# Performance work log

Measured on AMD Instinct MI355X. Metric: run time of the kernel, lower is better.

## Reference

```python
import jax, jax.numpy as jnp
import numpy as np

B, S, E, H, DQ = 8, 1024, 128, 8, 128  # batch, seq, embedding_dim, head_num, qkv_dim
HD = H * DQ  # 1024


def setup_inputs() -> dict:
    key = jax.random.key(0)
    ks = jax.random.split(key, 8)
    q = jax.random.normal(ks[0], (B, S, E), dtype=jnp.float32)
    k = jax.random.normal(ks[1], (B, S, E), dtype=jnp.float32)
    v = jax.random.normal(ks[2], (B, S, E), dtype=jnp.float32)
    mask = jnp.zeros((B, S), dtype=jnp.float32)  # rank2 ninf mask (additive)
    scale = 0.02
    Wq = jax.random.normal(ks[3], (HD, E), dtype=jnp.float32) * scale  # torch Linear weight [out,in]
    Wk = jax.random.normal(ks[4], (HD, E), dtype=jnp.float32) * scale
    Wv = jax.random.normal(ks[5], (HD, E), dtype=jnp.float32) * scale
    Wc = jax.random.normal(ks[6], (E, HD), dtype=jnp.float32) * scale
    bc = jax.random.normal(ks[7], (E,), dtype=jnp.float32) * scale
    return {"q": q, "k": k, "v": v, "mask": mask,
            "Wq": Wq, "Wk": Wk, "Wv": Wv, "Wc": Wc, "bc": bc}


def reference(q, k, v, mask, Wq, Wk, Wv, Wc, bc):
    batch, n, emb = q.shape
    hd = Wq.shape[0]
    # Faithful to source quirk: head_num recomputed as out_features // in_features
    head_num = hd // emb
    BIG = 1e9
    EPS = 1e-12

    def heads(x):  # [B, n, HD] -> [B, H, n, d]
        return x.reshape(batch, -1, head_num, hd // head_num).transpose(0, 2, 1, 3)

    qh = heads(q @ Wq.T)
    kh = heads(k @ Wk.T)
    vh = heads(v @ Wv.T)
    d = qh.shape[-1]

    score = jnp.einsum('bhnd,bhmd->bhnm', qh, kh) / jnp.sqrt(jnp.float32(d))
    score = score + mask[:, None, None, :]
    score = jnp.nan_to_num(score, nan=-BIG, posinf=BIG, neginf=-BIG)
    w = jax.nn.softmax(score, axis=-1)
    w = jnp.nan_to_num(w, nan=0.0, posinf=0.0, neginf=0.0)
    w = jnp.maximum(w, 0.0)
    row_sum = jnp.sum(w, axis=-1, keepdims=True)
    # zero-row fallback: replace fully-masked rows with tiny uniform weights
    w = jnp.where(row_sum <= 0.0, EPS, w)
    row_sum = jnp.sum(w, axis=-1, keepdims=True)
    w = w / (row_sum + EPS)

    out = jnp.einsum('bhnm,bhmd->bhnd', w, vh)  # [B,H,n,d]
    out_concat = out.transpose(0, 2, 1, 3).reshape(batch, n, hd)
    return out_concat @ Wc.T + bc
```

## Files before the change

kernel.cpp:

```cpp
#include <hip/hip_runtime.h>

typedef __bf16 bf16;
typedef __attribute__((ext_vector_type(8))) __bf16 bf16x8;
typedef __attribute__((ext_vector_type(4))) __bf16 bf16x4;
typedef __attribute__((ext_vector_type(4))) float f32x4;

constexpr int Bb = 8;
constexpr int Ss = 1024;
constexpr int Ee = 128;
constexpr int Hh = 8;
constexpr int Dd = 128;
constexpr int HD = 1024;

__device__ __forceinline__ void gl_lds16(const bf16* gp, bf16* lp) {
    __builtin_amdgcn_global_load_lds(
        (const __attribute__((address_space(1))) unsigned int*)gp,
        (__attribute__((address_space(3))) unsigned int*)lp, 16, 0, 0);
}

__global__ void k_cvt(const float* __restrict__ Wq, const float* __restrict__ Wk,
                      const float* __restrict__ Wv,
                      bf16* __restrict__ Wqb, bf16* __restrict__ Wkb, bf16* __restrict__ Wvb)
{
    int gid = blockIdx.x * 256 + threadIdx.x;
    const float* src; bf16* dst; int off; float s = 1.0f;
    if      (gid < 32768) { src = Wq; dst = Wqb; off = gid;         s = 0.12751741530603157f; }
    else if (gid < 65536) { src = Wk; dst = Wkb; off = gid - 32768; }
    else                  { src = Wv; dst = Wvb; off = gid - 65536; }
    float4 f = ((const float4*)src)[off];
    bf16x4 p;
    p[0] = (bf16)(f.x * s); p[1] = (bf16)(f.y * s);
    p[2] = (bf16)(f.z * s); p[3] = (bf16)(f.w * s);
    ((bf16x4*)dst)[off] = p;
}

__global__ __launch_bounds__(256, 2) void k_qkv(
    const float* __restrict__ qin, const float* __restrict__ kin, const float* __restrict__ vin,
    const bf16* __restrict__ Wqb, const bf16* __restrict__ Wkb, const bf16* __restrict__ Wvb,
    bf16* __restrict__ Qh, bf16* __restrict__ Kh, bf16* __restrict__ Vt)
{
    const int rb    = blockIdx.x;
    const int h     = blockIdx.y;
    const int which = blockIdx.z;
    const float* x = (which == 0) ? qin : (which == 1) ? kin : vin;
    const bf16*  W = (which == 0) ? Wqb : (which == 1) ? Wkb : Wvb;

    __shared__ bf16 Xs[128][136];
    __shared__ bf16 Ws[128][136];

    const int tid  = threadIdx.x;
    const int wv   = tid >> 6;
    const int lane = tid & 63;
    const int lo   = lane & 15;
    const int q4   = lane >> 4;

#pragma unroll
    for (int t = 0; t < 8; ++t) {
        int c = tid + t * 256;
        int row = c >> 4, c8 = (c & 15) << 3;
        const float* xp = &x[(rb * 128 + row) * Ee + c8];
        float4 f0 = *(const float4*)xp;
        float4 f1 = *(const float4*)(xp + 4);
        bf16x8 p;
        p[0] = (bf16)f0.x; p[1] = (bf16)f0.y; p[2] = (bf16)f0.z; p[3] = (bf16)f0.w;
        p[4] = (bf16)f1.x; p[5] = (bf16)f1.y; p[6] = (bf16)f1.z; p[7] = (bf16)f1.w;
        *(bf16x8*)&Xs[row][c8] = p;
        *(bf16x8*)&Ws[row][c8] = *(const bf16x8*)&W[(h * 128 + row) * Ee + c8];
    }
    __syncthreads();

    const bf16 (*Ap)[136] = (which == 2) ? Ws : Xs;
    const bf16 (*Bp)[136] = (which == 2) ? Xs : Ws;

    f32x4 acc[2][8];
#pragma unroll
    for (int i = 0; i < 2; ++i)
#pragma unroll
        for (int j = 0; j < 8; ++j) acc[i][j] = f32x4{0.f, 0.f, 0.f, 0.f};

#pragma unroll
    for (int kq = 0; kq < 4; ++kq) {
        bf16x8 a[2], b8[8];
#pragma unroll
        for (int ri = 0; ri < 2; ++ri)
            a[ri] = *(const bf16x8*)&Ap[wv * 32 + ri * 16 + lo][kq * 32 + q4 * 8];
#pragma unroll
        for (int cj = 0; cj < 8; ++cj)
            b8[cj] = *(const bf16x8*)&Bp[cj * 16 + lo][kq * 32 + q4 * 8];
#pragma unroll
        for (int ri = 0; ri < 2; ++ri)
#pragma unroll
            for (int cj = 0; cj < 8; ++cj)
                acc[ri][cj] = __builtin_amdgcn_mfma_f32_16x16x32_bf16(
                    a[ri], b8[cj], acc[ri][cj], 0, 0, 0);
    }

    const int bb = rb >> 3;
    const int s0 = (rb & 7) * 128;
    if (which < 2) {
        bf16* dst = ((which == 0) ? Qh : Kh) + (bb * Hh + h) * Ss * Dd;
#pragma unroll
        for (int ri = 0; ri < 2; ++ri)
#pragma unroll
            for (int cj = 0; cj < 8; ++cj)
#pragma unroll
                for (int r = 0; r < 4; ++r) {
                    int row = wv * 32 + ri * 16 + q4 * 4 + r;
                    int col = cj * 16 + lo;
                    dst[(s0 + row) * Dd + col] = (bf16)acc[ri][cj][r];
                }
    } else {
        bf16* dst = Vt + (bb * Hh + h) * Dd * Ss;
#pragma unroll
        for (int ri = 0; ri < 2; ++ri)
#pragma unroll
            for (int cj = 0; cj < 8; ++cj)
#pragma unroll
                for (int r = 0; r < 4; ++r) {
                    int row = wv * 32 + ri * 16 + q4 * 4 + r;
                    int col = cj * 16 + lo;
                    dst[row * Ss + s0 + col] = (bf16)acc[ri][cj][r];
                }
    }
}

__global__ __launch_bounds__(512, 2) void k_attn(
    const bf16* __restrict__ Qh, const bf16* __restrict__ Kh, const bf16* __restrict__ Vt,
    const float* __restrict__ mask, bf16* __restrict__ oc)
{
    const int bh = blockIdx.x;
    const int qg = blockIdx.y;
    const int b  = bh >> 3;
    const int h  = bh & 7;
    const int tid  = threadIdx.x;
    const int wv   = tid >> 6;
    const int lane = tid & 63;
    const int lo   = lane & 15;
    const int q4   = lane >> 4;

    __shared__ bf16 KsL[2][64 * 128];
    __shared__ bf16 VsL[2][128 * 64];
    __shared__ float maskS[1024];

    const bf16* Qb = Qh + bh * Ss * Dd;
    const bf16* Kb = Kh + bh * Ss * Dd;
    const bf16* Vb = Vt + bh * Dd * Ss;

    auto stage = [&](int bi, int j0) {
#pragma unroll
        for (int t = 0; t < 2; ++t) {
            int i = wv * 2 + t;
            int row = i * 4 + (lane >> 4);
            int grow = (row & 32) + (((row >> 2) & 3) << 3)
                     + (((row >> 4) & 1) << 2) + (row & 3);
            int g = (lane & 15) ^ (row & 7);
            gl_lds16(Kb + (j0 + grow) * Dd + g * 8, &KsL[bi][i * 512]);
        }
#pragma unroll
        for (int t = 0; t < 2; ++t) {
            int i = wv * 2 + t;
            int row = i * 8 + (lane >> 3);
            int g = (lane & 7) ^ (row & 7);
            gl_lds16(Vb + row * Ss + j0 + g * 8, &VsL[bi][i * 512]);
        }
    };

    stage(0, 0);

#pragma unroll
    for (int t = 0; t < 2; ++t)
        maskS[tid + t * 512] = mask[b * Ss + tid + t * 512] * 1.4426950408889634f;

    const int q0 = qg * 256 + wv * 32;
    bf16x8 qf[2][4];
#pragma unroll
    for (int nt = 0; nt < 2; ++nt)
#pragma unroll
        for (int kq = 0; kq < 4; ++kq)
            qf[nt][kq] = *(const bf16x8*)&Qb[(q0 + nt * 16 + lo) * Dd + kq * 32 + q4 * 8];

    f32x4 accO[8][2];
#pragma unroll
    for (int dm = 0; dm < 8; ++dm)
#pragma unroll
        for (int nt = 0; nt < 2; ++nt) accO[dm][nt] = f32x4{0.f, 0.f, 0.f, 0.f};
    float lsum[2] = {0.f, 0.f};

    const int sw = lo & 7;

#pragma unroll 2
    for (int kt = 0; kt < 16; ++kt) {
        const int bi = kt & 1;
        const int j0 = kt * 64;
        __syncthreads();
        if (kt < 15) stage(bi ^ 1, j0 + 64);

        f32x4 sc[4][2];
#pragma unroll
        for (int c = 0; c < 4; ++c)
#pragma unroll
            for (int nt = 0; nt < 2; ++nt) sc[c][nt] = f32x4{0.f, 0.f, 0.f, 0.f};
#pragma unroll
        for (int kq = 0; kq < 4; ++kq) {
            bf16x8 kf[4];
#pragma unroll
            for (int c = 0; c < 4; ++c)
                kf[c] = *(const bf16x8*)&KsL[bi][(c * 16 + lo) * 128 + (((kq << 2) + q4) ^ sw) * 8];
#pragma unroll
            for (int c = 0; c < 4; ++c)
#pragma unroll
                for (int nt = 0; nt < 2; ++nt)
                    sc[c][nt] = __builtin_amdgcn_mfma_f32_16x16x32_bf16(
                        kf[c], qf[nt][kq], sc[c][nt], 0, 0, 0);
        }

        bf16x8 p8[2][2];
#pragma unroll
        for (int kb = 0; kb < 2; ++kb) {
#pragma unroll
            for (int t = 0; t < 2; ++t) {
                const float4 mv = *(const float4*)&maskS[j0 + kb * 32 + q4 * 8 + t * 4];
                const int c = kb * 2 + t;
#pragma unroll
                for (int nt = 0; nt < 2; ++nt) {
                    float e0 = exp2f(sc[c][nt][0] + mv.x);
                    float e1 = exp2f(sc[c][nt][1] + mv.y);
                    float e2 = exp2f(sc[c][nt][2] + mv.z);
                    float e3 = exp2f(sc[c][nt][3] + mv.w);
                    lsum[nt] += (e0 + e1) + (e2 + e3);
                    p8[kb][nt][t * 4 + 0] = (bf16)e0;
                    p8[kb][nt][t * 4 + 1] = (bf16)e1;
                    p8[kb][nt][t * 4 + 2] = (bf16)e2;
                    p8[kb][nt][t * 4 + 3] = (bf16)e3;
                }
            }
        }

#pragma unroll
        for (int kb = 0; kb < 2; ++kb)
#pragma unroll
            for (int dm = 0; dm < 8; ++dm) {
                bf16x8 vf = *(const bf16x8*)&VsL[bi][(dm * 16 + lo) * 64 + (((kb << 2) + q4) ^ sw) * 8];
#pragma unroll
                for (int nt = 0; nt < 2; ++nt)
                    accO[dm][nt] = __builtin_amdgcn_mfma_f32_16x16x32_bf16(
                        vf, p8[kb][nt], accO[dm][nt], 0, 0, 0);
            }
    }

#pragma unroll
    for (int nt = 0; nt < 2; ++nt) {
        float s = lsum[nt];
        s += __shfl_xor(s, 16, 64);
        s += __shfl_xor(s, 32, 64);
        float inv = 1.0f / (s + 1e-12f);
        int sg = q0 + nt * 16 + lo;
        bf16* dst = oc + (b * Ss + sg) * HD + h * 128;
#pragma unroll
        for (int dm = 0; dm < 8; ++dm) {
            bf16x4 o;
#pragma unroll
            for (int r = 0; r < 4; ++r) o[r] = (bf16)(accO[dm][nt][r] * inv);
            *(bf16x4*)&dst[dm * 16 + q4 * 4] = o;
        }
    }
}

__global__ __launch_bounds__(256, 4) void k_proj(
    const bf16* __restrict__ oc, const float* __restrict__ Wc,
    const float* __restrict__ bc, float* __restrict__ out)
{
    const int mt   = blockIdx.x;
    const int tid  = threadIdx.x;
    const int wv   = tid >> 6;
    const int lane = tid & 63;
    const int lo   = lane & 15;
    const int q4   = lane >> 4;

    f32x4 acc[2];
    acc[0] = f32x4{0.f, 0.f, 0.f, 0.f};
    acc[1] = f32x4{0.f, 0.f, 0.f, 0.f};

    const bf16* arow = oc + (mt * 16 + lo) * HD + q4 * 8;

    for (int kc = 0; kc < 8; ++kc) {
        const int k0 = kc * 128;
        bf16x8 a[4];
#pragma unroll
        for (int kq = 0; kq < 4; ++kq)
            a[kq] = *(const bf16x8*)&arow[k0 + kq * 32];
#pragma unroll
        for (int cj = 0; cj < 2; ++cj) {
            const int n = wv * 32 + cj * 16 + lo;
#pragma unroll
            for (int kq = 0; kq < 4; ++kq) {
                const float* wp = &Wc[n * HD + k0 + kq * 32 + q4 * 8];
                float4 f0 = *(const float4*)wp;
                float4 f1 = *(const float4*)(wp + 4);
                bf16x8 bfr;
                bfr[0] = (bf16)f0.x; bfr[1] = (bf16)f0.y; bfr[2] = (bf16)f0.z; bfr[3] = (bf16)f0.w;
                bfr[4] = (bf16)f1.x; bfr[5] = (bf16)f1.y; bfr[6] = (bf16)f1.z; bfr[7] = (bf16)f1.w;
                acc[cj] = __builtin_amdgcn_mfma_f32_16x16x32_bf16(
                    a[kq], bfr, acc[cj], 0, 0, 0);
            }
        }
    }

#pragma unroll
    for (int cj = 0; cj < 2; ++cj) {
        int col = wv * 32 + cj * 16 + lo;
        float bias = bc[col];
#pragma unroll
        for (int r = 0; r < 4; ++r) {
            int row = mt * 16 + q4 * 4 + r;
            out[row * Ee + col] = acc[cj][r] + bias;
        }
    }
}

extern "C" void kernel_launch(void* const* d_in, const int* in_sizes, int n_in,
                              void* d_out, int out_size, void* d_ws, size_t ws_size,
                              hipStream_t stream)
{
    const float* q    = (const float*)d_in[0];
    const float* k    = (const float*)d_in[1];
    const float* v    = (const float*)d_in[2];
    const float* mask = (const float*)d_in[3];
    const float* Wq   = (const float*)d_in[4];
    const float* Wk   = (const float*)d_in[5];
    const float* Wv   = (const float*)d_in[6];
    const float* Wc   = (const float*)d_in[7];
    const float* bc   = (const float*)d_in[8];
    float* out = (float*)d_out;

    constexpr int NBH = Bb * Hh * Ss * Dd;
    bf16* Qh = (bf16*)d_ws;
    bf16* Kh = Qh + NBH;
    bf16* Vt = Kh + NBH;
    bf16* oc = Vt + NBH;
    bf16* Wqb = oc;
    bf16* Wkb = Wqb + HD * Ee;
    bf16* Wvb = Wkb + HD * Ee;

    k_cvt<<<dim3(384), 256, 0, stream>>>(Wq, Wk, Wv, Wqb, Wkb, Wvb);
    k_qkv<<<dim3(64, 8, 3), 256, 0, stream>>>(q, k, v, Wqb, Wkb, Wvb, Qh, Kh, Vt);
    k_attn<<<dim3(64, 4), 512, 0, stream>>>(Qh, Kh, Vt, mask, oc);
    k_proj<<<dim3(512), 256, 0, stream>>>(oc, Wc, bc, out);
}
```

Before: 178.4 us.

## Shrink attention blocks to 2 waves and 32-key tiles with new LDS swizzle

Restructures the attention kernel from 512-thread blocks covering 256 queries to 128-thread blocks covering 64 queries, launching 1024 blocks instead of 256. Key/value tiles shrink from 64 to 32 keys per iteration, giving 32 iterations, with a new XOR swizzle pattern and precomputed staging offsets. The aim is more blocks in flight across CUs and less LDS per block. In exchange, each K/V tile is reused by fewer waves, so global traffic for K/V rises fourfold, and there are twice as many barriers per block.

```diff
diff --git a/kernel.cpp b/kernel.cpp
--- a/kernel.cpp
+++ b/kernel.cpp
@@ -124,7 +124,7 @@
     }
 }
 
-__global__ __launch_bounds__(512, 2) void k_attn(
+__global__ __launch_bounds__(128, 2) void k_attn(
     const bf16* __restrict__ Qh, const bf16* __restrict__ Kh, const bf16* __restrict__ Vt,
     const float* __restrict__ mask, bf16* __restrict__ oc)
 {
@@ -138,40 +138,43 @@
     const int lo   = lane & 15;
     const int q4   = lane >> 4;
 
-    __shared__ bf16 KsL[2][64 * 128];
-    __shared__ bf16 VsL[2][128 * 64];
+    __shared__ bf16 KsL[2][32 * 128];
+    __shared__ bf16 VsL[2][128 * 32];
     __shared__ float maskS[1024];
 
     const bf16* Qb = Qh + bh * Ss * Dd;
     const bf16* Kb = Kh + bh * Ss * Dd;
     const bf16* Vb = Vt + bh * Dd * Ss;
 
+    int koff[4], voff[4];
+#pragma unroll
+    for (int t = 0; t < 4; ++t) {
+        int i = wv * 4 + t;
+        int rho  = i * 4 + (lane >> 4);
+        int kap  = 8 * ((rho >> 2) & 3) + 4 * ((rho >> 4) & 1) + (rho & 3);
+        int sK   = ((((rho >> 1) ^ (rho >> 3)) & 1) << 2) | (((rho >> 2) & 1) << 3);
+        int gK   = (lane & 15) ^ sK;
+        koff[t]  = kap * Dd + gK * 8;
+        int vrow = i * 16 + (lane >> 2);
+        voff[t]  = vrow * Ss + (lane & 3) * 8;
+    }
+
     auto stage = [&](int bi, int j0) {
 #pragma unroll
-        for (int t = 0; t < 2; ++t) {
-            int i = wv * 2 + t;
-            int row = i * 4 + (lane >> 4);
-            int grow = (row & 32) + (((row >> 2) & 3) << 3)
-                     + (((row >> 4) & 1) << 2) + (row & 3);
-            int g = (lane & 15) ^ (row & 7);
-            gl_lds16(Kb + (j0 + grow) * Dd + g * 8, &KsL[bi][i * 512]);
-        }
-#pragma unroll
-        for (int t = 0; t < 2; ++t) {
-            int i = wv * 2 + t;
-            int row = i * 8 + (lane >> 3);
-            int g = (lane & 7) ^ (row & 7);
-            gl_lds16(Vb + row * Ss + j0 + g * 8, &VsL[bi][i * 512]);
-        }
+        for (int t = 0; t < 4; ++t)
+            gl_lds16(Kb + j0 * Dd + koff[t], &KsL[bi][(wv * 4 + t) * 512]);
+#pragma unroll
+        for (int t = 0; t < 4; ++t)
+            gl_lds16(Vb + j0 + voff[t], &VsL[bi][(wv * 4 + t) * 512]);
     };
 
     stage(0, 0);
 
 #pragma unroll
-    for (int t = 0; t < 2; ++t)
-        maskS[tid + t * 512] = mask[b * Ss + tid + t * 512] * 1.4426950408889634f;
-
-    const int q0 = qg * 256 + wv * 32;
+    for (int t = 0; t < 8; ++t)
+        maskS[tid + t * 128] = mask[b * Ss + tid + t * 128] * 1.4426950408889634f;
+
+    const int q0 = qg * 64 + wv * 32;
     bf16x8 qf[2][4];
 #pragma unroll
     for (int nt = 0; nt < 2; ++nt)
@@ -186,66 +189,60 @@
         for (int nt = 0; nt < 2; ++nt) accO[dm][nt] = f32x4{0.f, 0.f, 0.f, 0.f};
     float lsum[2] = {0.f, 0.f};
 
-    const int sw = lo & 7;
+    const int sw2 = ((((lo >> 1) ^ (lo >> 3)) & 1) << 2) | (((lo >> 2) & 1) << 3);
 
 #pragma unroll 2
-    for (int kt = 0; kt < 16; ++kt) {
+    for (int kt = 0; kt < 32; ++kt) {
         const int bi = kt & 1;
-        const int j0 = kt * 64;
+        const int j0 = kt * 32;
         __syncthreads();
-        if (kt < 15) stage(bi ^ 1, j0 + 64);
-
-        f32x4 sc[4][2];
-#pragma unroll
-        for (int c = 0; c < 4; ++c)
+        if (kt < 31) stage(bi ^ 1, j0 + 32);
+
+        f32x4 sc[2][2];
+#pragma unroll
+        for (int c = 0; c < 2; ++c)
 #pragma unroll
             for (int nt = 0; nt < 2; ++nt) sc[c][nt] = f32x4{0.f, 0.f, 0.f, 0.f};
 #pragma unroll
         for (int kq = 0; kq < 4; ++kq) {
-            bf16x8 kf[4];
-#pragma unroll
-            for (int c = 0; c < 4; ++c)
-                kf[c] = *(const bf16x8*)&KsL[bi][(c * 16 + lo) * 128 + (((kq << 2) + q4) ^ sw) * 8];
-#pragma unroll
-            for (int c = 0; c < 4; ++c)
+            bf16x8 kf[2];
+#pragma unroll
+            for (int c = 0; c < 2; ++c)
+                kf[c] = *(const bf16x8*)&KsL[bi][(c * 16 + lo) * 128 + (((kq << 2) | q4) ^ sw2) * 8];
+#pragma unroll
+            for (int c = 0; c < 2; ++c)
 #pragma unroll
                 for (int nt = 0; nt < 2; ++nt)
                     sc[c][nt] = __builtin_amdgcn_mfma_f32_16x16x32_bf16(
                         kf[c], qf[nt][kq], sc[c][nt], 0, 0, 0);
         }
 
-        bf16x8 p8[2][2];
-#pragma unroll
-        for (int kb = 0; kb < 2; ++kb) {
-#pragma unroll
-            for (int t = 0; t < 2; ++t) {
-                const float4 mv = *(const float4*)&maskS[j0 + kb * 32 + q4 * 8 + t * 4];
-                const int c = kb * 2 + t;
-#pragma unroll
-                for (int nt = 0; nt < 2; ++nt) {
-                    float e0 = exp2f(sc[c][nt][0] + mv.x);
-                    float e1 = exp2f(sc[c][nt][1] + mv.y);
-                    float e2 = exp2f(sc[c][nt][2] + mv.z);
-                    float e3 = exp2f(sc[c][nt][3] + mv.w);
-                    lsum[nt] += (e0 + e1) + (e2 + e3);
-                    p8[kb][nt][t * 4 + 0] = (bf16)e0;
-                    p8[kb][nt][t * 4 + 1] = (bf16)e1;
-                    p8[kb][nt][t * 4 + 2] = (bf16)e2;
-                    p8[kb][nt][t * 4 + 3] = (bf16)e3;
-                }
+        bf16x8 p8[2];
+#pragma unroll
+        for (int c = 0; c < 2; ++c) {
+            const float4 mv = *(const float4*)&maskS[j0 + q4 * 8 + c * 4];
+#pragma unroll
+            for (int nt = 0; nt < 2; ++nt) {
+                float e0 = exp2f(sc[c][nt][0] + mv.x);
+                float e1 = exp2f(sc[c][nt][1] + mv.y);
+                float e2 = exp2f(sc[c][nt][2] + mv.z);
+                float e3 = exp2f(sc[c][nt][3] + mv.w);
+                lsum[nt] += (e0 + e1) + (e2 + e3);
+                p8[nt][c * 4 + 0] = (bf16)e0;
+                p8[nt][c * 4 + 1] = (bf16)e1;
+                p8[nt][c * 4 + 2] = (bf16)e2;
+                p8[nt][c * 4 + 3] = (bf16)e3;
             }
         }
 
 #pragma unroll
-        for (int kb = 0; kb < 2; ++kb)
-#pragma unroll
-            for (int dm = 0; dm < 8; ++dm) {
-                bf16x8 vf = *(const bf16x8*)&VsL[bi][(dm * 16 + lo) * 64 + (((kb << 2) + q4) ^ sw) * 8];
-#pragma unroll
-                for (int nt = 0; nt < 2; ++nt)
-                    accO[dm][nt] = __builtin_amdgcn_mfma_f32_16x16x32_bf16(
-                        vf, p8[kb][nt], accO[dm][nt], 0, 0, 0);
-            }
+        for (int dm = 0; dm < 8; ++dm) {
+            bf16x8 vf = *(const bf16x8*)&VsL[bi][(dm * 16 + lo) * 32 + q4 * 8];
+#pragma unroll
+            for (int nt = 0; nt < 2; ++nt)
+                accO[dm][nt] = __builtin_amdgcn_mfma_f32_16x16x32_bf16(
+                    vf, p8[nt], accO[dm][nt], 0, 0, 0);
+        }
     }
 
 #pragma unroll
@@ -344,6 +341,6 @@
 
     k_cvt<<<dim3(384), 256, 0, stream>>>(Wq, Wk, Wv, Wqb, Wkb, Wvb);
     k_qkv<<<dim3(64, 8, 3), 256, 0, stream>>>(q, k, v, Wqb, Wkb, Wvb, Qh, Kh, Vt);
-    k_attn<<<dim3(64, 4), 512, 0, stream>>>(Qh, Kh, Vt, mask, oc);
+    k_attn<<<dim3(64, 16), 128, 0, stream>>>(Qh, Kh, Vt, mask, oc);
     k_proj<<<dim3(512), 256, 0, stream>>>(oc, Wc, bc, out);
 }
```

After: 181.3 us. Within noise of the previous version (+1.7%).

## Pre-convert activations to bf16, async-load QKV tiles, double-step attention pipeline

Applied to the files above, without the earlier changes.

The conversion kernel now also casts the q/k/v activations to bf16, so the projection kernel can fill shared memory with swizzled direct global-to-LDS loads instead of converting floats in registers. The attention kernel grows its K/V staging to four buffers, prefetches two tiles ahead and issues one barrier per pair of tiles, which cuts synchronisation and hides more load latency. In exchange it adds an extra pass over the activations in global memory and uses roughly 132KB of LDS per attention block, which limits residency to one block per CU.

```diff
diff --git a/kernel.cpp b/kernel.cpp
--- a/kernel.cpp
+++ b/kernel.cpp
@@ -18,15 +18,20 @@
         (__attribute__((address_space(3))) unsigned int*)lp, 16, 0, 0);
 }
 
-__global__ void k_cvt(const float* __restrict__ Wq, const float* __restrict__ Wk,
-                      const float* __restrict__ Wv,
+__global__ void k_cvt(const float* __restrict__ q, const float* __restrict__ k,
+                      const float* __restrict__ v, const float* __restrict__ Wq,
+                      const float* __restrict__ Wk, const float* __restrict__ Wv,
+                      bf16* __restrict__ xq, bf16* __restrict__ xk, bf16* __restrict__ xv,
                       bf16* __restrict__ Wqb, bf16* __restrict__ Wkb, bf16* __restrict__ Wvb)
 {
     int gid = blockIdx.x * 256 + threadIdx.x;
     const float* src; bf16* dst; int off; float s = 1.0f;
-    if      (gid < 32768) { src = Wq; dst = Wqb; off = gid;         s = 0.12751741530603157f; }
-    else if (gid < 65536) { src = Wk; dst = Wkb; off = gid - 32768; }
-    else                  { src = Wv; dst = Wvb; off = gid - 65536; }
+    if      (gid < 262144) { src = q;  dst = xq;  off = gid; }
+    else if (gid < 524288) { src = k;  dst = xk;  off = gid - 262144; }
+    else if (gid < 786432) { src = v;  dst = xv;  off = gid - 524288; }
+    else if (gid < 819200) { src = Wq; dst = Wqb; off = gid - 786432; s = 0.12751741530603157f; }
+    else if (gid < 851968) { src = Wk; dst = Wkb; off = gid - 819200; }
+    else                   { src = Wv; dst = Wvb; off = gid - 851968; }
     float4 f = ((const float4*)src)[off];
     bf16x4 p;
     p[0] = (bf16)(f.x * s); p[1] = (bf16)(f.y * s);
@@ -35,18 +40,18 @@
 }
 
 __global__ __launch_bounds__(256, 2) void k_qkv(
-    const float* __restrict__ qin, const float* __restrict__ kin, const float* __restrict__ vin,
+    const bf16* __restrict__ xq, const bf16* __restrict__ xk, const bf16* __restrict__ xv,
     const bf16* __restrict__ Wqb, const bf16* __restrict__ Wkb, const bf16* __restrict__ Wvb,
     bf16* __restrict__ Qh, bf16* __restrict__ Kh, bf16* __restrict__ Vt)
 {
     const int rb    = blockIdx.x;
     const int h     = blockIdx.y;
     const int which = blockIdx.z;
-    const float* x = (which == 0) ? qin : (which == 1) ? kin : vin;
-    const bf16*  W = (which == 0) ? Wqb : (which == 1) ? Wkb : Wvb;
-
-    __shared__ bf16 Xs[128][136];
-    __shared__ bf16 Ws[128][136];
+    const bf16* x = (which == 0) ? xq  : (which == 1) ? xk  : xv;
+    const bf16* W = (which == 0) ? Wqb : (which == 1) ? Wkb : Wvb;
+
+    __shared__ bf16 Xs[128 * 128];
+    __shared__ bf16 Ws[128 * 128];
 
     const int tid  = threadIdx.x;
     const int wv   = tid >> 6;
@@ -56,21 +61,17 @@
 
 #pragma unroll
     for (int t = 0; t < 8; ++t) {
-        int c = tid + t * 256;
-        int row = c >> 4, c8 = (c & 15) << 3;
-        const float* xp = &x[(rb * 128 + row) * Ee + c8];
-        float4 f0 = *(const float4*)xp;
-        float4 f1 = *(const float4*)(xp + 4);
-        bf16x8 p;
-        p[0] = (bf16)f0.x; p[1] = (bf16)f0.y; p[2] = (bf16)f0.z; p[3] = (bf16)f0.w;
-        p[4] = (bf16)f1.x; p[5] = (bf16)f1.y; p[6] = (bf16)f1.z; p[7] = (bf16)f1.w;
-        *(bf16x8*)&Xs[row][c8] = p;
-        *(bf16x8*)&Ws[row][c8] = *(const bf16x8*)&W[(h * 128 + row) * Ee + c8];
+        int i = wv * 8 + t;
+        int row = i * 4 + (lane >> 4);
+        int g = (lane & 15) ^ (row & 7);
+        gl_lds16(x + (rb * 128 + row) * Ee + g * 8, &Xs[i * 512]);
+        gl_lds16(W + (h * 128 + row) * Ee + g * 8, &Ws[i * 512]);
     }
     __syncthreads();
 
-    const bf16 (*Ap)[136] = (which == 2) ? Ws : Xs;
-    const bf16 (*Bp)[136] = (which == 2) ? Xs : Ws;
+    const bf16* Ap = (which == 2) ? Ws : Xs;
+    const bf16* Bp = (which == 2) ? Xs : Ws;
+    const int sw = lo & 7;
 
     f32x4 acc[2][8];
 #pragma unroll
@@ -80,13 +81,14 @@
 
 #pragma unroll
     for (int kq = 0; kq < 4; ++kq) {
+        const int ch = (((kq << 2) + q4) ^ sw) * 8;
         bf16x8 a[2], b8[8];
 #pragma unroll
         for (int ri = 0; ri < 2; ++ri)
-            a[ri] = *(const bf16x8*)&Ap[wv * 32 + ri * 16 + lo][kq * 32 + q4 * 8];
+            a[ri] = *(const bf16x8*)&Ap[(wv * 32 + ri * 16 + lo) * 128 + ch];
 #pragma unroll
         for (int cj = 0; cj < 8; ++cj)
-            b8[cj] = *(const bf16x8*)&Bp[cj * 16 + lo][kq * 32 + q4 * 8];
+            b8[cj] = *(const bf16x8*)&Bp[(cj * 16 + lo) * 128 + ch];
 #pragma unroll
         for (int ri = 0; ri < 2; ++ri)
 #pragma unroll
@@ -138,8 +140,8 @@
     const int lo   = lane & 15;
     const int q4   = lane >> 4;
 
-    __shared__ bf16 KsL[2][64 * 128];
-    __shared__ bf16 VsL[2][128 * 64];
+    __shared__ bf16 KsL[4][64 * 128];
+    __shared__ bf16 VsL[4][128 * 64];
     __shared__ float maskS[1024];
 
     const bf16* Qb = Qh + bh * Ss * Dd;
@@ -166,6 +168,7 @@
     };
 
     stage(0, 0);
+    stage(1, 64);
 
 #pragma unroll
     for (int t = 0; t < 2; ++t)
@@ -188,13 +191,7 @@
 
     const int sw = lo & 7;
 
-#pragma unroll 2
-    for (int kt = 0; kt < 16; ++kt) {
-        const int bi = kt & 1;
-        const int j0 = kt * 64;
-        __syncthreads();
-        if (kt < 15) stage(bi ^ 1, j0 + 64);
-
+    auto compute = [&](int bi, int j0) {
         f32x4 sc[4][2];
 #pragma unroll
         for (int c = 0; c < 4; ++c)
@@ -246,6 +243,17 @@
                     accO[dm][nt] = __builtin_amdgcn_mfma_f32_16x16x32_bf16(
                         vf, p8[kb][nt], accO[dm][nt], 0, 0, 0);
             }
+    };
+
+    for (int w = 0; w < 8; ++w) {
+        const int t0 = 2 * w;
+        __syncthreads();
+        if (w < 7) {
+            stage((t0 + 2) & 3, (t0 + 2) * 64);
+            stage((t0 + 3) & 3, (t0 + 3) * 64);
+        }
+        compute(t0 & 3, t0 * 64);
+        compute((t0 + 1) & 3, (t0 + 1) * 64);
     }
 
 #pragma unroll
@@ -333,17 +341,21 @@
     const float* bc   = (const float*)d_in[8];
     float* out = (float*)d_out;
 
-    constexpr int NBH = Bb * Hh * Ss * Dd;
+    constexpr int NBH = Bb * Ss * Dd * Hh / Hh * Hh;
     bf16* Qh = (bf16*)d_ws;
-    bf16* Kh = Qh + NBH;
-    bf16* Vt = Kh + NBH;
-    bf16* oc = Vt + NBH;
-    bf16* Wqb = oc;
+    bf16* Kh = Qh + 8388608;
+    bf16* Vt = Kh + 8388608;
+    bf16* oc = Vt + 8388608;
+    bf16* xq  = oc;
+    bf16* xk  = xq + Bb * Ss * Ee;
+    bf16* xv  = xk + Bb * Ss * Ee;
+    bf16* Wqb = xv + Bb * Ss * Ee;
     bf16* Wkb = Wqb + HD * Ee;
     bf16* Wvb = Wkb + HD * Ee;
-
-    k_cvt<<<dim3(384), 256, 0, stream>>>(Wq, Wk, Wv, Wqb, Wkb, Wvb);
-    k_qkv<<<dim3(64, 8, 3), 256, 0, stream>>>(q, k, v, Wqb, Wkb, Wvb, Qh, Kh, Vt);
+    (void)NBH; (void)in_sizes; (void)n_in; (void)out_size; (void)ws_size;
+
+    k_cvt<<<dim3(3456), 256, 0, stream>>>(q, k, v, Wq, Wk, Wv, xq, xk, xv, Wqb, Wkb, Wvb);
+    k_qkv<<<dim3(64, 8, 3), 256, 0, stream>>>(xq, xk, xv, Wqb, Wkb, Wvb, Qh, Kh, Vt);
     k_attn<<<dim3(64, 4), 512, 0, stream>>>(Qh, Kh, Vt, mask, oc);
     k_proj<<<dim3(512), 256, 0, stream>>>(oc, Wc, bc, out);
 }
```

Result: no change. 177.7 us (-0.4%).
